# Optimization experiments

Hardware: AMD Instinct MI355X
Metric: run time of the kernel (lower is better)

## Reference

```python
import jax, jax.numpy as jnp
import numpy as np

B, L, D, H = 2, 2048, 1024, 16
HD = D // H

def setup_inputs() -> dict:
    key = jax.random.key(0)
    ks = jax.random.split(key, 9)
    s = 1.0 / np.sqrt(D)
    return {
        "x": jax.random.normal(ks[0], (B, L, D), jnp.float32),
        "Wq": jax.random.normal(ks[1], (D, D), jnp.float32) * s,
        "bq": jax.random.normal(ks[2], (D,), jnp.float32) * 0.02,
        "Wk": jax.random.normal(ks[3], (D, D), jnp.float32) * s,
        "bk": jax.random.normal(ks[4], (D,), jnp.float32) * 0.02,
        "Wv": jax.random.normal(ks[5], (D, D), jnp.float32) * s,
        "bv": jax.random.normal(ks[6], (D,), jnp.float32) * 0.02,
        "Wo": jax.random.normal(ks[7], (D, D), jnp.float32) * s,
        "bo": jax.random.normal(ks[8], (D,), jnp.float32) * 0.02,
    }

def reference(x, Wq, bq, Wk, bk, Wv, bv, Wo, bo):
    b, l, d = x.shape
    # projections -> [B, H, L, HD]
    def split_heads(t):
        return t.reshape(b, l, H, HD).transpose(0, 2, 1, 3)
    Q = split_heads(x @ Wq + bq)
    K = split_heads(x @ Wk + bk)
    V = split_heads(x @ Wv + bv)
    scores = jnp.einsum('bhqd,bhkd->bhqk', Q, K)  # [B,H,L,L]
    causal = jnp.tril(jnp.ones((l, l), bool))
    scores = jnp.where(causal, scores, -jnp.inf)
    attn = jax.nn.softmax(scores / np.sqrt(HD), axis=-1)
    ctx = jnp.einsum('bhqk,bhkd->bhqd', attn, V)
    ctx = ctx.transpose(0, 2, 1, 3).reshape(b, l, d)
    return ctx @ Wo + bo
```

## Files before the change

kernel.cpp:

```cpp
#include <hip/hip_runtime.h>
#include <stdint.h>

typedef unsigned short u16;
typedef __attribute__((ext_vector_type(8))) __bf16 bf16x8;
typedef __attribute__((ext_vector_type(4))) float f32x4;
typedef __attribute__((ext_vector_type(16))) float f32x16;

__device__ __forceinline__ u16 f2bf(float f) {
  union { float f; uint32_t u; } c; c.f = f;
  uint32_t u = c.u + 0x7fffu + ((c.u >> 16) & 1u);
  return (u16)(u >> 16);
}
__device__ __forceinline__ uint32_t cvtpk(float a, float b) {
  uint32_t r;
  asm("v_cvt_pk_bf16_f32 %0, %1, %2" : "=v"(r) : "v"(a), "v"(b));
  return r;
}

__device__ __forceinline__ void async16(const u16* g, u16* l) {
  __builtin_amdgcn_global_load_lds(
      (const __attribute__((address_space(1))) void*)g,
      (__attribute__((address_space(3))) void*)l, 16, 0, 0);
}

__device__ __forceinline__ f32x4 mfma16(bf16x8 a, bf16x8 b, f32x4 c) {
  return __builtin_amdgcn_mfma_f32_16x16x32_bf16(a, b, c, 0, 0, 0);
}
__device__ __forceinline__ f32x16 mfma32(bf16x8 a, bf16x8 b, f32x16 c) {
  return __builtin_amdgcn_mfma_f32_32x32x16_bf16(a, b, c, 0, 0, 0);
}


__global__ __launch_bounds__(256) void x_cvt_kernel(const float* __restrict__ x,
                                                    u16* __restrict__ xb) {
  int i = (blockIdx.x * 256 + threadIdx.x) * 4;
  float4 v = *(const float4*)(x + i);
  uint2 t; t.x = cvtpk(v.x, v.y); t.y = cvtpk(v.z, v.w);
  *(uint2*)(xb + i) = t;
}

__global__ __launch_bounds__(256) void wt_cvt_kernel(const float* __restrict__ Wq,
                                                     const float* __restrict__ Wk,
                                                     const float* __restrict__ Wv,
                                                     const float* __restrict__ Wo,
                                                     u16* __restrict__ out) {
  __shared__ __align__(16) u16 t[64][72];
  int z = blockIdx.z;
  const float* W = (z == 0) ? Wq : (z == 1) ? Wk : (z == 2) ? Wv : Wo;
  u16* o = out + (size_t)z * (1u << 20);
  int n0 = blockIdx.x * 64, k0 = blockIdx.y * 64;
  int tid = threadIdx.x;
  int c4 = (tid & 15) * 4, r0 = tid >> 4;
#pragma unroll
  for (int i = 0; i < 4; i++) {
    int r = r0 + i * 16;
    float4 v = *(const float4*)(W + (size_t)(k0 + r) * 1024 + n0 + c4);
    t[c4 + 0][r] = f2bf(v.x);
    t[c4 + 1][r] = f2bf(v.y);
    t[c4 + 2][r] = f2bf(v.z);
    t[c4 + 3][r] = f2bf(v.w);
  }
  __syncthreads();
  int n = tid >> 2, kc = (tid & 3) * 16;
  uint4 a = *(const uint4*)&t[n][kc];
  uint4 b = *(const uint4*)&t[n][kc + 8];
  *(uint4*)(o + (size_t)(n0 + n) * 1024 + k0 + kc) = a;
  *(uint4*)(o + (size_t)(n0 + n) * 1024 + k0 + kc + 8) = b;
}

template <int TN>
__device__ __forceinline__ void gemm_core2(const u16* __restrict__ A,
                                           const u16* __restrict__ Bt,
                                           u16* As, u16* Bs,
                                           f32x4 (&acc)[4][TN / 32]) {
  constexpr int NJ = TN / 32;
  constexpr int ASZ = 128 * 32, BSZ = TN * 32;
  const int tid = threadIdx.x, wave = tid >> 6, lane = tid & 63;
  const int low = lane & 15, hi = lane >> 4;
  const int wm = wave >> 1, wn = wave & 1;
  const int m0 = blockIdx.y * 128, n0 = blockIdx.x * TN;
  const f32x4 fzero = {0.f, 0.f, 0.f, 0.f};
#pragma unroll
  for (int i = 0; i < 4; i++)
#pragma unroll
    for (int j = 0; j < NJ; j++) acc[i][j] = fzero;

  const int ea0 = wave * 128 + lane, ea1 = ea0 + 64;
  const u16* ga0 = A + (size_t)(m0 + (ea0 >> 2)) * 1024 + (ea0 & 3) * 8;
  const u16* ga1 = A + (size_t)(m0 + (ea1 >> 2)) * 1024 + (ea1 & 3) * 8;
  u16* la0 = As + (wave * 2 + 0) * 512;
  u16* la1 = As + (wave * 2 + 1) * 512;

  const int eb0 = (TN == 128) ? (wave * 128 + lane) : (wave * 64 + lane);
  const int eb1 = eb0 + 64;
  const u16* gb0 = Bt + (size_t)(n0 + (eb0 >> 2)) * 1024 + (eb0 & 3) * 8;
  const u16* gb1 = Bt + (size_t)(n0 + (eb1 >> 2)) * 1024 + (eb1 & 3) * 8;
  u16* lb0 = Bs + ((TN == 128) ? (wave * 2 + 0) * 512 : wave * 512);
  u16* lb1 = Bs + (wave * 2 + 1) * 512;

  const u16* ap = As + (wm * 64 + low) * 32 + hi * 8;
  const u16* bp = Bs + (wn * (TN / 2) + low) * 32 + hi * 8;

#define GSTAGE(buf, KT)                                                        \
  {                                                                            \
    async16(ga0 + (KT), la0 + (buf) * ASZ);                                    \
    async16(ga1 + (KT), la1 + (buf) * ASZ);                                    \
    async16(gb0 + (KT), lb0 + (buf) * BSZ);                                    \
    if (TN == 128) async16(gb1 + (KT), lb1 + (buf) * BSZ);                     \
  }

  GSTAGE(0, 0)
  __syncthreads();
  int buf = 0;
  for (int kt = 0; kt < 1024; kt += 32) {
    if (kt + 32 < 1024) GSTAGE(buf ^ 1, kt + 32)
    bf16x8 af[4], bfv[NJ];
#pragma unroll
    for (int i = 0; i < 4; i++)
      af[i] = *(const bf16x8*)(ap + buf * ASZ + i * 16 * 32);
#pragma unroll
    for (int j = 0; j < NJ; j++)
      bfv[j] = *(const bf16x8*)(bp + buf * BSZ + j * 16 * 32);
#pragma unroll
    for (int i = 0; i < 4; i++)
#pragma unroll
      for (int j = 0; j < NJ; j++) acc[i][j] = mfma16(af[i], bfv[j], acc[i][j]);
    __syncthreads();
    buf ^= 1;
  }
#undef GSTAGE
}

__global__ __launch_bounds__(256) void gemm_qkv_kernel(
    const u16* __restrict__ xb, const u16* __restrict__ wT,
    const float* __restrict__ bq, const float* __restrict__ bk,
    const float* __restrict__ bv,
    u16* __restrict__ qs, u16* __restrict__ ks, u16* __restrict__ vts) {
  __shared__ __align__(16) u16 smem[17440];
  u16* As = smem;
  u16* Bs = smem + 8192;
  const int z = blockIdx.z;
  const u16* Bt = wT + (size_t)z * (1u << 20);
  f32x4 acc[4][4];
  gemm_core2<128>(xb, Bt, As, Bs, acc);

  const float* bias = (z == 0) ? bq : (z == 1) ? bk : bv;
  u16* out = (z == 0) ? qs : (z == 1) ? ks : vts;
  const float scale = (z == 0) ? 0.180336880f : 1.0f;
  const int tid = threadIdx.x, wave = tid >> 6, lane = tid & 63;
  const int low = lane & 15, hi = lane >> 4;
  const int wm = wave >> 1, wn = wave & 1;
  const int m0 = blockIdx.y * 128, n0 = blockIdx.x * 128;

  const int h = (n0 >> 6) + wn;
  const int gmb = m0 + wm * 64;
  const int b = gmb >> 11;
  const int lb = gmb & 2047;

  u16* tile = smem + wave * 4360;
#pragma unroll
  for (int i = 0; i < 4; i++)
#pragma unroll
    for (int j = 0; j < 4; j++) {
      int hd = j * 16 + low;
      float bval = bias[h * 64 + hd];
#pragma unroll
      for (int r = 0; r < 4; r++) {
        int row = i * 16 + hi * 4 + r;
        tile[row * 68 + hd] = f2bf((acc[i][j][r] + bval) * scale);
      }
    }

  if (z != 2) {
    u16* dst = out + ((size_t)((b * 16 + h) * 2048 + lb + lane)) * 64;
    const u16* src = tile + lane * 68;
#pragma unroll
    for (int c = 0; c < 4; c++) {
      uint2 a0 = *(const uint2*)(src + c * 16 + 0);
      uint2 a1 = *(const uint2*)(src + c * 16 + 4);
      uint2 a2 = *(const uint2*)(src + c * 16 + 8);
      uint2 a3 = *(const uint2*)(src + c * 16 + 12);
      uint4 w0; w0.x = a0.x; w0.y = a0.y; w0.z = a1.x; w0.w = a1.y;
      uint4 w1; w1.x = a2.x; w1.y = a2.y; w1.z = a3.x; w1.w = a3.y;
      *(uint4*)(dst + c * 16 + 0) = w0;
      *(uint4*)(dst + c * 16 + 8) = w1;
    }
  } else {
    int l4 = (lane & 15) * 4;
    int lp4 = (l4 & ~12) | ((l4 & 4) << 1) | ((l4 & 8) >> 1);
    int ghd = lane >> 4;
    u16* vbase = out + ((size_t)(b * 16 + h) * 64) * 2048 + lb + lp4;
#pragma unroll
    for (int s = 0; s < 16; s++) {
      int hd = s * 4 + ghd;
      uint32_t v0 = tile[(l4 + 0) * 68 + hd];
      uint32_t v1 = tile[(l4 + 1) * 68 + hd];
      uint32_t v2 = tile[(l4 + 2) * 68 + hd];
      uint32_t v3 = tile[(l4 + 3) * 68 + hd];
      uint2 w; w.x = v0 | (v1 << 16); w.y = v2 | (v3 << 16);
      *(uint2*)(vbase + (size_t)hd * 2048) = w;
    }
  }
}

__global__ __launch_bounds__(256) void gemm_out_kernel(
    const u16* __restrict__ ctx, const u16* __restrict__ woT,
    const float* __restrict__ bo, float* __restrict__ out) {
  __shared__ __align__(16) u16 As[2 * 128 * 32];
  __shared__ __align__(16) u16 Bs[2 * 64 * 32];
  f32x4 acc[4][2];
  gemm_core2<64>(ctx, woT, As, Bs, acc);
  const int tid = threadIdx.x, wave = tid >> 6, lane = tid & 63;
  const int low = lane & 15, hi = lane >> 4;
  const int wm = wave >> 1, wn = wave & 1;
  const int m0 = blockIdx.y * 128, n0 = blockIdx.x * 64;
#pragma unroll
  for (int i = 0; i < 4; i++)
#pragma unroll
    for (int j = 0; j < 2; j++) {
      int gn = n0 + wn * 32 + j * 16 + low;
      float bval = bo[gn];
#pragma unroll
      for (int r = 0; r < 4; r++) {
        int gm = m0 + wm * 64 + i * 16 + hi * 4 + r;
        out[(size_t)gm * 1024 + gn] = acc[i][j][r] + bval;
      }
    }
}

__global__ __launch_bounds__(512) void flash_kernel(
    const u16* __restrict__ Qs, const u16* __restrict__ Ks,
    const u16* __restrict__ Vts, u16* __restrict__ ctx) {
  __shared__ __align__(16) u16 Kls[2][2][64 * 64];
  __shared__ __align__(16) u16 Vls[2][2][64 * 64];

  const int bid = blockIdx.x;
  const int qt = (bid < 256) ? (15 - (bid >> 5)) : ((bid - 256) >> 5);
  const int bh = bid & 31;
  const int qb = qt * 128;
  const int nT = qt + 1;

  const int tid = threadIdx.x, wave = tid >> 6, lane = tid & 63;
  const int wq = wave & 3, g = wave >> 2;
  const int q32 = lane & 31, hi2 = lane >> 5;
  const int x7 = q32 & 7;

  const u16* Qb = Qs + (size_t)bh * (2048 * 64);
  const u16* Kb = Ks + (size_t)bh * (2048 * 64);
  const u16* Vb = Vts + (size_t)bh * (64 * 2048);

  const int qrow = qb + wq * 32 + q32;
  bf16x8 qf[4];
#pragma unroll
  for (int ds = 0; ds < 4; ds++)
    qf[ds] = *(const bf16x8*)(Qb + (size_t)qrow * 64 + ds * 16 + hi2 * 8);

  f32x16 o0, o1;
#pragma unroll
  for (int r = 0; r < 16; r++) { o0[r] = 0.f; o1[r] = 0.f; }
  float m_ = -1e30f, l_ = 0.f;

#define STAGE(buf, KT0)                                                        \
  {                                                                            \
    _Pragma("unroll") for (int i = 0; i < 2; i++) {                            \
      int row = (wq * 2 + i) * 8 + (lane >> 3);                                \
      async16(Kb + (size_t)((KT0) + row) * 64 +                                \
                  (((lane & 7) ^ (row & 7)) * 8),                              \
              &Kls[g][buf][(wq * 2 + i) * 512]);                               \
      async16(Vb + (size_t)row * 2048 + (KT0) +                                \
                  (((lane & 7) ^ (row & 7)) * 8),                              \
              &Vls[g][buf][(wq * 2 + i) * 512]);                               \
    }                                                                          \
  }

  const int tb = g * nT;
  STAGE(0, (tb + 0) * 64)
  STAGE(1, (tb + 1) * 64)

  const int qmax = qb + wq * 32 + 31;

  int cur = 0;
  for (int t = 0; t < nT; t++) {
    const int kt0 = (tb + t) * 64;
    if (t + 1 < nT) { asm volatile("s_waitcnt vmcnt(4)" ::: "memory"); }
    else            { asm volatile("s_waitcnt vmcnt(0)" ::: "memory"); }
    __builtin_amdgcn_s_barrier();

    if (kt0 <= qmax) {
      const u16* Kc = &Kls[g][cur][0];
      const u16* Vc = &Vls[g][cur][0];

      f32x16 s0, s1;
#pragma unroll
      for (int r = 0; r < 16; r++) { s0[r] = 0.f; s1[r] = 0.f; }
      __builtin_amdgcn_s_setprio(1);
#pragma unroll
      for (int ds = 0; ds < 4; ds++) {
        int cs = ((ds * 2 + hi2) ^ x7) * 8;
        bf16x8 kf0 = *(const bf16x8*)(Kc + q32 * 64 + cs);
        bf16x8 kf1 = *(const bf16x8*)(Kc + (32 + q32) * 64 + cs);
        s0 = mfma32(kf0, qf[ds], s0);
        s1 = mfma32(kf1, qf[ds], s1);
      }
      __builtin_amdgcn_s_setprio(0);

      bf16x8 vf0[4], vf1[4];
#pragma unroll
      for (int ksx = 0; ksx < 4; ksx++) {
        int sc = ((2 * ksx + hi2) ^ x7) * 8;
        vf0[ksx] = *(const bf16x8*)(Vc + q32 * 64 + sc);
        vf1[ksx] = *(const bf16x8*)(Vc + (32 + q32) * 64 + sc);
      }

      if (kt0 + 63 > qb + wq * 32) {
#pragma unroll
        for (int r = 0; r < 16; r++) {
          int kl = (r & 3) + 8 * (r >> 2) + 4 * hi2;
          if (kt0 + kl > qrow) s0[r] = -1e30f;
          if (kt0 + 32 + kl > qrow) s1[r] = -1e30f;
        }
      }

      float pm = -1e30f;
#pragma unroll
      for (int r = 0; r < 16; r++) pm = fmaxf(pm, fmaxf(s0[r], s1[r]));
      pm = fmaxf(pm, __shfl_xor(pm, 32));
      if (__any(pm > m_ + 8.f)) {
        float mn = fmaxf(m_, pm);
        float corr = __builtin_amdgcn_exp2f(m_ - mn);
        m_ = mn;
        l_ *= corr;
#pragma unroll
        for (int r = 0; r < 16; r++) { o0[r] *= corr; o1[r] *= corr; }
      }

      float rs = 0.f;
#pragma unroll
      for (int r = 0; r < 16; r++) {
        s0[r] = __builtin_amdgcn_exp2f(s0[r] - m_);
        s1[r] = __builtin_amdgcn_exp2f(s1[r] - m_);
        rs += s0[r] + s1[r];
      }
      rs += __shfl_xor(rs, 32);
      l_ += rs;

      bf16x8 pb[4];
#pragma unroll
      for (int ksx = 0; ksx < 4; ksx++) {
        union { uint32_t u[4]; bf16x8 v; } pu;
        if (ksx < 2) {
          int rb = 8 * ksx;
          pu.u[0] = cvtpk(s0[rb + 0], s0[rb + 1]);
          pu.u[1] = cvtpk(s0[rb + 2], s0[rb + 3]);
          pu.u[2] = cvtpk(s0[rb + 4], s0[rb + 5]);
          pu.u[3] = cvtpk(s0[rb + 6], s0[rb + 7]);
        } else {
          int rb = 8 * (ksx - 2);
          pu.u[0] = cvtpk(s1[rb + 0], s1[rb + 1]);
          pu.u[1] = cvtpk(s1[rb + 2], s1[rb + 3]);
          pu.u[2] = cvtpk(s1[rb + 4], s1[rb + 5]);
          pu.u[3] = cvtpk(s1[rb + 6], s1[rb + 7]);
        }
        pb[ksx] = pu.v;
      }

      __builtin_amdgcn_s_setprio(1);
#pragma unroll
      for (int ksx = 0; ksx < 4; ksx++) {
        o0 = mfma32(vf0[ksx], pb[ksx], o0);
        o1 = mfma32(vf1[ksx], pb[ksx], o1);
      }
      __builtin_amdgcn_s_setprio(0);
    }

    __builtin_amdgcn_s_barrier();
    if (t + 2 < nT) STAGE(cur, (tb + t + 2) * 64)
    cur ^= 1;
  }

  __syncthreads();
  float* mb = (float*)&Kls[0][0][0] + wq * 2304;
  if (g == 1) {
#pragma unroll
    for (int m = 0; m < 4; m++) {
      f32x4 qa = {o0[4 * m + 0], o0[4 * m + 1], o0[4 * m + 2], o0[4 * m + 3]};
      f32x4 qb2 = {o1[4 * m + 0], o1[4 * m + 1], o1[4 * m + 2], o1[4 * m + 3]};
      *(f32x4*)(mb + m * 256 + (lane << 2)) = qa;
      *(f32x4*)(mb + (4 + m) * 256 + (lane << 2)) = qb2;
    }
    mb[2048 + (lane << 1) + 0] = m_;
    mb[2048 + (lane << 1) + 1] = l_;
  }
  __syncthreads();
  if (g == 0) {
    float m1 = mb[2048 + (lane << 1) + 0];
    float l1 = mb[2048 + (lane << 1) + 1];
    float mm = fmaxf(m_, m1);
    float cA = __builtin_amdgcn_exp2f(m_ - mm);
    float cB = __builtin_amdgcn_exp2f(m1 - mm);
    l_ = l_ * cA + l1 * cB;
#pragma unroll
    for (int m = 0; m < 4; m++) {
      f32x4 qa = *(const f32x4*)(mb + m * 256 + (lane << 2));
      f32x4 qb2 = *(const f32x4*)(mb + (4 + m) * 256 + (lane << 2));
#pragma unroll
      for (int j = 0; j < 4; j++) {
        o0[4 * m + j] = o0[4 * m + j] * cA + qa[j] * cB;
        o1[4 * m + j] = o1[4 * m + j] * cA + qb2[j] * cB;
      }
    }

    const int b = bh >> 4, h = bh & 15;
    float inv = 1.f / l_;
    size_t base = ((size_t)(b * 2048 + qrow)) * 1024 + h * 64;
#pragma unroll
    for (int m = 0; m < 4; m++) {
      uint2 w0, w1;
      w0.x = cvtpk(o0[4 * m + 0] * inv, o0[4 * m + 1] * inv);
      w0.y = cvtpk(o0[4 * m + 2] * inv, o0[4 * m + 3] * inv);
      *(uint2*)(ctx + base + 8 * m + 4 * hi2) = w0;
      w1.x = cvtpk(o1[4 * m + 0] * inv, o1[4 * m + 1] * inv);
      w1.y = cvtpk(o1[4 * m + 2] * inv, o1[4 * m + 3] * inv);
      *(uint2*)(ctx + base + 32 + 8 * m + 4 * hi2) = w1;
    }
  }
}


extern "C" void kernel_launch(void* const* d_in, const int* in_sizes, int n_in,
                              void* d_out, int out_size, void* d_ws, size_t ws_size,
                              hipStream_t stream) {
  const float* x  = (const float*)d_in[0];
  const float* Wq = (const float*)d_in[1];
  const float* bq = (const float*)d_in[2];
  const float* Wk = (const float*)d_in[3];
  const float* bk = (const float*)d_in[4];
  const float* Wv = (const float*)d_in[5];
  const float* bv = (const float*)d_in[6];
  const float* Wo = (const float*)d_in[7];
  const float* bo = (const float*)d_in[8];

  char* ws = (char*)d_ws;
  u16* xb  = (u16*)(ws);
  u16* wT  = (u16*)(ws + (8u << 20));
  u16* qs  = (u16*)(ws + (16u << 20));
  u16* ks  = (u16*)(ws + (24u << 20));
  u16* vts = (u16*)(ws + (32u << 20));
  u16* ctx = (u16*)(ws + (40u << 20));

  x_cvt_kernel<<<4096, 256, 0, stream>>>(x, xb);
  wt_cvt_kernel<<<dim3(16, 16, 4), 256, 0, stream>>>(Wq, Wk, Wv, Wo, wT);
  gemm_qkv_kernel<<<dim3(8, 32, 3), 256, 0, stream>>>(xb, wT, bq, bk, bv, qs, ks, vts);
  flash_kernel<<<512, 512, 0, stream>>>(qs, ks, vts, ctx);
  gemm_out_kernel<<<dim3(16, 32), 256, 0, stream>>>(ctx, wT + 3 * (1u << 20), bo, (float*)d_out);
}
```

Measured before the change: 118.4 us.

## Split flash attention KV range across four wave groups with 1024-thread blocks

Doubles the flash kernel block to 1024 threads so four wave groups split each query tile's KV tiles, instead of two groups taking contiguous halves. Tiles are assigned round-robin, and out-of-range prefetches are clamped to the last tile. Partial outputs from groups 1-3 are merged into group 0 through shared memory. The per-tile row-sum cross-lane shuffle is deferred to the end, max and sum use tree reductions, and the block order for the second half of the grid changes. The aim is more parallelism per query tile and a shorter serial KV loop. The cost is a larger LDS footprint, a tighter per-thread register budget at 1024 threads, and a bigger final merge.

```diff
diff --git a/kernel.cpp b/kernel.cpp
--- a/kernel.cpp
+++ b/kernel.cpp
@@ -228,17 +228,17 @@
     }
 }
 
-__global__ __launch_bounds__(512) void flash_kernel(
+__global__ __launch_bounds__(1024) void flash_kernel(
     const u16* __restrict__ Qs, const u16* __restrict__ Ks,
     const u16* __restrict__ Vts, u16* __restrict__ ctx) {
-  __shared__ __align__(16) u16 Kls[2][2][64 * 64];
-  __shared__ __align__(16) u16 Vls[2][2][64 * 64];
+  __shared__ __align__(16) u16 smem[65536];
 
   const int bid = blockIdx.x;
-  const int qt = (bid < 256) ? (15 - (bid >> 5)) : ((bid - 256) >> 5);
+  const int qt = (bid < 256) ? (15 - (bid >> 5)) : (7 - ((bid - 256) >> 5));
   const int bh = bid & 31;
   const int qb = qt * 128;
-  const int nT = qt + 1;
+  const int nkv = 2 * qt + 2;
+  const int loopN = (nkv + 3) >> 2;
 
   const int tid = threadIdx.x, wave = tid >> 6, lane = tid & 63;
   const int wq = wave & 3, g = wave >> 2;
@@ -259,6 +259,9 @@
 #pragma unroll
   for (int r = 0; r < 16; r++) { o0[r] = 0.f; o1[r] = 0.f; }
   float m_ = -1e30f, l_ = 0.f;
+
+  u16* Kg = smem + g * 8192;
+  u16* Vg = smem + 32768 + g * 8192;
 
 #define STAGE(buf, KT0)                                                        \
   {                                                                            \
@@ -266,29 +269,33 @@
       int row = (wq * 2 + i) * 8 + (lane >> 3);                                \
       async16(Kb + (size_t)((KT0) + row) * 64 +                                \
                   (((lane & 7) ^ (row & 7)) * 8),                              \
-              &Kls[g][buf][(wq * 2 + i) * 512]);                               \
+              Kg + (buf) * 4096 + (wq * 2 + i) * 512);                         \
       async16(Vb + (size_t)row * 2048 + (KT0) +                                \
                   (((lane & 7) ^ (row & 7)) * 8),                              \
-              &Vls[g][buf][(wq * 2 + i) * 512]);                               \
+              Vg + (buf) * 4096 + (wq * 2 + i) * 512);                         \
     }                                                                          \
   }
 
-  const int tb = g * nT;
-  STAGE(0, (tb + 0) * 64)
-  STAGE(1, (tb + 1) * 64)
+  const int Tmax = nkv - 1;
+  {
+    int T0 = (g < nkv) ? g : Tmax;
+    int T1 = (4 + g < nkv) ? (4 + g) : Tmax;
+    STAGE(0, T0 * 64)
+    STAGE(1, T1 * 64)
+  }
 
   const int qmax = qb + wq * 32 + 31;
 
   int cur = 0;
-  for (int t = 0; t < nT; t++) {
-    const int kt0 = (tb + t) * 64;
-    if (t + 1 < nT) { asm volatile("s_waitcnt vmcnt(4)" ::: "memory"); }
-    else            { asm volatile("s_waitcnt vmcnt(0)" ::: "memory"); }
+  for (int t = 0; t < loopN; t++) {
+    const int kt0 = (4 * t + g) * 64;
+    if (t + 1 < loopN) { asm volatile("s_waitcnt vmcnt(4)" ::: "memory"); }
+    else               { asm volatile("s_waitcnt vmcnt(0)" ::: "memory"); }
     __builtin_amdgcn_s_barrier();
 
     if (kt0 <= qmax) {
-      const u16* Kc = &Kls[g][cur][0];
-      const u16* Vc = &Vls[g][cur][0];
+      const u16* Kc = Kg + cur * 4096;
+      const u16* Vc = Vg + cur * 4096;
 
       f32x16 s0, s1;
 #pragma unroll
@@ -321,9 +328,15 @@
         }
       }
 
-      float pm = -1e30f;
-#pragma unroll
-      for (int r = 0; r < 16; r++) pm = fmaxf(pm, fmaxf(s0[r], s1[r]));
+      float t16[16];
+#pragma unroll
+      for (int r = 0; r < 16; r++) t16[r] = fmaxf(s0[r], s1[r]);
+#pragma unroll
+      for (int w = 8; w >= 1; w >>= 1)
+#pragma unroll
+        for (int i = 0; i < 8; i++)
+          if (i < w) t16[i] = fmaxf(t16[i], t16[i + w]);
+      float pm = t16[0];
       pm = fmaxf(pm, __shfl_xor(pm, 32));
       if (__any(pm > m_ + 8.f)) {
         float mn = fmaxf(m_, pm);
@@ -334,15 +347,19 @@
         for (int r = 0; r < 16; r++) { o0[r] *= corr; o1[r] *= corr; }
       }
 
-      float rs = 0.f;
+      float a16[16];
 #pragma unroll
       for (int r = 0; r < 16; r++) {
         s0[r] = __builtin_amdgcn_exp2f(s0[r] - m_);
         s1[r] = __builtin_amdgcn_exp2f(s1[r] - m_);
-        rs += s0[r] + s1[r];
-      }
-      rs += __shfl_xor(rs, 32);
-      l_ += rs;
+        a16[r] = s0[r] + s1[r];
+      }
+#pragma unroll
+      for (int w = 8; w >= 1; w >>= 1)
+#pragma unroll
+        for (int i = 0; i < 8; i++)
+          if (i < w) a16[i] += a16[i + w];
+      l_ += a16[0];
 
       bf16x8 pb[4];
 #pragma unroll
@@ -374,13 +391,17 @@
     }
 
     __builtin_amdgcn_s_barrier();
-    if (t + 2 < nT) STAGE(cur, (tb + t + 2) * 64)
+    if (t + 2 < loopN) {
+      int Tn = 4 * (t + 2) + g;
+      if (Tn > Tmax) Tn = Tmax;
+      STAGE(cur, Tn * 64)
+    }
     cur ^= 1;
   }
 
   __syncthreads();
-  float* mb = (float*)&Kls[0][0][0] + wq * 2304;
-  if (g == 1) {
+  float* mb = (float*)smem + (wq * 3 + (g - 1)) * 2176;
+  if (g >= 1) {
 #pragma unroll
     for (int m = 0; m < 4; m++) {
       f32x4 qa = {o0[4 * m + 0], o0[4 * m + 1], o0[4 * m + 2], o0[4 * m + 3]};
@@ -393,25 +414,31 @@
   }
   __syncthreads();
   if (g == 0) {
-    float m1 = mb[2048 + (lane << 1) + 0];
-    float l1 = mb[2048 + (lane << 1) + 1];
-    float mm = fmaxf(m_, m1);
-    float cA = __builtin_amdgcn_exp2f(m_ - mm);
-    float cB = __builtin_amdgcn_exp2f(m1 - mm);
-    l_ = l_ * cA + l1 * cB;
-#pragma unroll
-    for (int m = 0; m < 4; m++) {
-      f32x4 qa = *(const f32x4*)(mb + m * 256 + (lane << 2));
-      f32x4 qb2 = *(const f32x4*)(mb + (4 + m) * 256 + (lane << 2));
-#pragma unroll
-      for (int j = 0; j < 4; j++) {
-        o0[4 * m + j] = o0[4 * m + j] * cA + qa[j] * cB;
-        o1[4 * m + j] = o1[4 * m + j] * cA + qb2[j] * cB;
-      }
-    }
-
+#pragma unroll
+    for (int gs = 1; gs < 4; gs++) {
+      float* ms = (float*)smem + (wq * 3 + (gs - 1)) * 2176;
+      float m1 = ms[2048 + (lane << 1) + 0];
+      float l1 = ms[2048 + (lane << 1) + 1];
+      float mm = fmaxf(m_, m1);
+      float cA = __builtin_amdgcn_exp2f(m_ - mm);
+      float cB = __builtin_amdgcn_exp2f(m1 - mm);
+      m_ = mm;
+      l_ = l_ * cA + l1 * cB;
+#pragma unroll
+      for (int m = 0; m < 4; m++) {
+        f32x4 qa = *(const f32x4*)(ms + m * 256 + (lane << 2));
+        f32x4 qb2 = *(const f32x4*)(ms + (4 + m) * 256 + (lane << 2));
+#pragma unroll
+        for (int j = 0; j < 4; j++) {
+          o0[4 * m + j] = o0[4 * m + j] * cA + qa[j] * cB;
+          o1[4 * m + j] = o1[4 * m + j] * cA + qb2[j] * cB;
+        }
+      }
+    }
+
+    float lrow = l_ + __shfl_xor(l_, 32);
     const int b = bh >> 4, h = bh & 15;
-    float inv = 1.f / l_;
+    float inv = 1.f / lrow;
     size_t base = ((size_t)(b * 2048 + qrow)) * 1024 + h * 64;
 #pragma unroll
     for (int m = 0; m < 4; m++) {
@@ -451,6 +478,6 @@
   x_cvt_kernel<<<4096, 256, 0, stream>>>(x, xb);
   wt_cvt_kernel<<<dim3(16, 16, 4), 256, 0, stream>>>(Wq, Wk, Wv, Wo, wT);
   gemm_qkv_kernel<<<dim3(8, 32, 3), 256, 0, stream>>>(xb, wT, bq, bk, bv, qs, ks, vts);
-  flash_kernel<<<512, 512, 0, stream>>>(qs, ks, vts, ctx);
+  flash_kernel<<<512, 1024, 0, stream>>>(qs, ks, vts, ctx);
   gemm_out_kernel<<<dim3(16, 32), 256, 0, stream>>>(ctx, wT + 3 * (1u << 20), bo, (float*)d_out);
 }
```

Result: slower. 141.5 us (+19.5%).

## Load K and V tiles straight from global memory, dropping LDS double buffering

Applied to the files above, without the earlier changes.

Removes the async global-to-LDS staging of K and V tiles, along with the double buffer, waitcnt and barriers. Each wave now reads its K rows and V^T rows directly from global memory into registers. Because no barriers remain in the loop, waves can exit as soon as their causal range ends. The trade-off is that the four q-waves of each group each read the same K/V tile separately from global/L2, with no async prefetch to hide the latency.

```diff
diff --git a/kernel.cpp b/kernel.cpp
--- a/kernel.cpp
+++ b/kernel.cpp
@@ -231,8 +231,7 @@
 __global__ __launch_bounds__(512) void flash_kernel(
     const u16* __restrict__ Qs, const u16* __restrict__ Ks,
     const u16* __restrict__ Vts, u16* __restrict__ ctx) {
-  __shared__ __align__(16) u16 Kls[2][2][64 * 64];
-  __shared__ __align__(16) u16 Vls[2][2][64 * 64];
+  __shared__ __align__(16) float msc[4][2304];
 
   const int bid = blockIdx.x;
   const int qt = (bid < 256) ? (15 - (bid >> 5)) : ((bid - 256) >> 5);
@@ -243,7 +242,6 @@
   const int tid = threadIdx.x, wave = tid >> 6, lane = tid & 63;
   const int wq = wave & 3, g = wave >> 2;
   const int q32 = lane & 31, hi2 = lane >> 5;
-  const int x7 = q32 & 7;
 
   const u16* Qb = Qs + (size_t)bh * (2048 * 64);
   const u16* Kb = Ks + (size_t)bh * (2048 * 64);
@@ -260,126 +258,103 @@
   for (int r = 0; r < 16; r++) { o0[r] = 0.f; o1[r] = 0.f; }
   float m_ = -1e30f, l_ = 0.f;
 
-#define STAGE(buf, KT0)                                                        \
-  {                                                                            \
-    _Pragma("unroll") for (int i = 0; i < 2; i++) {                            \
-      int row = (wq * 2 + i) * 8 + (lane >> 3);                                \
-      async16(Kb + (size_t)((KT0) + row) * 64 +                                \
-                  (((lane & 7) ^ (row & 7)) * 8),                              \
-              &Kls[g][buf][(wq * 2 + i) * 512]);                               \
-      async16(Vb + (size_t)row * 2048 + (KT0) +                                \
-                  (((lane & 7) ^ (row & 7)) * 8),                              \
-              &Vls[g][buf][(wq * 2 + i) * 512]);                               \
-    }                                                                          \
-  }
-
   const int tb = g * nT;
-  STAGE(0, (tb + 0) * 64)
-  STAGE(1, (tb + 1) * 64)
-
   const int qmax = qb + wq * 32 + 31;
 
-  int cur = 0;
+  const u16* vr0 = Vb + (size_t)q32 * 2048;
+  const u16* vr1 = Vb + (size_t)(32 + q32) * 2048;
+
   for (int t = 0; t < nT; t++) {
     const int kt0 = (tb + t) * 64;
-    if (t + 1 < nT) { asm volatile("s_waitcnt vmcnt(4)" ::: "memory"); }
-    else            { asm volatile("s_waitcnt vmcnt(0)" ::: "memory"); }
-    __builtin_amdgcn_s_barrier();
-
-    if (kt0 <= qmax) {
-      const u16* Kc = &Kls[g][cur][0];
-      const u16* Vc = &Vls[g][cur][0];
-
-      f32x16 s0, s1;
-#pragma unroll
-      for (int r = 0; r < 16; r++) { s0[r] = 0.f; s1[r] = 0.f; }
-      __builtin_amdgcn_s_setprio(1);
-#pragma unroll
-      for (int ds = 0; ds < 4; ds++) {
-        int cs = ((ds * 2 + hi2) ^ x7) * 8;
-        bf16x8 kf0 = *(const bf16x8*)(Kc + q32 * 64 + cs);
-        bf16x8 kf1 = *(const bf16x8*)(Kc + (32 + q32) * 64 + cs);
-        s0 = mfma32(kf0, qf[ds], s0);
-        s1 = mfma32(kf1, qf[ds], s1);
+    if (kt0 > qmax) break;
+
+    const u16* kr0 = Kb + (size_t)(kt0 + q32) * 64;
+    const u16* kr1 = Kb + (size_t)(kt0 + 32 + q32) * 64;
+    f32x16 s0, s1;
+#pragma unroll
+    for (int r = 0; r < 16; r++) { s0[r] = 0.f; s1[r] = 0.f; }
+    __builtin_amdgcn_s_setprio(1);
+#pragma unroll
+    for (int ds = 0; ds < 4; ds++) {
+      int cs = (2 * ds + hi2) * 8;
+      bf16x8 kf0 = *(const bf16x8*)(kr0 + cs);
+      bf16x8 kf1 = *(const bf16x8*)(kr1 + cs);
+      s0 = mfma32(kf0, qf[ds], s0);
+      s1 = mfma32(kf1, qf[ds], s1);
+    }
+    __builtin_amdgcn_s_setprio(0);
+
+    bf16x8 vf0[4], vf1[4];
+#pragma unroll
+    for (int ksx = 0; ksx < 4; ksx++) {
+      int sc = (2 * ksx + hi2) * 8;
+      vf0[ksx] = *(const bf16x8*)(vr0 + kt0 + sc);
+      vf1[ksx] = *(const bf16x8*)(vr1 + kt0 + sc);
+    }
+
+    if (kt0 + 63 > qb + wq * 32) {
+#pragma unroll
+      for (int r = 0; r < 16; r++) {
+        int kl = (r & 3) + 8 * (r >> 2) + 4 * hi2;
+        if (kt0 + kl > qrow) s0[r] = -1e30f;
+        if (kt0 + 32 + kl > qrow) s1[r] = -1e30f;
       }
-      __builtin_amdgcn_s_setprio(0);
-
-      bf16x8 vf0[4], vf1[4];
-#pragma unroll
-      for (int ksx = 0; ksx < 4; ksx++) {
-        int sc = ((2 * ksx + hi2) ^ x7) * 8;
-        vf0[ksx] = *(const bf16x8*)(Vc + q32 * 64 + sc);
-        vf1[ksx] = *(const bf16x8*)(Vc + (32 + q32) * 64 + sc);
+    }
+
+    float pm = -1e30f;
+#pragma unroll
+    for (int r = 0; r < 16; r++) pm = fmaxf(pm, fmaxf(s0[r], s1[r]));
+    pm = fmaxf(pm, __shfl_xor(pm, 32));
+    if (__any(pm > m_ + 8.f)) {
+      float mn = fmaxf(m_, pm);
+      float corr = __builtin_amdgcn_exp2f(m_ - mn);
+      m_ = mn;
+      l_ *= corr;
+#pragma unroll
+      for (int r = 0; r < 16; r++) { o0[r] *= corr; o1[r] *= corr; }
+    }
+
+    float rs = 0.f;
+#pragma unroll
+    for (int r = 0; r < 16; r++) {
+      s0[r] = __builtin_amdgcn_exp2f(s0[r] - m_);
+      s1[r] = __builtin_amdgcn_exp2f(s1[r] - m_);
+      rs += s0[r] + s1[r];
+    }
+    rs += __shfl_xor(rs, 32);
+    l_ += rs;
+
+    bf16x8 pb[4];
+#pragma unroll
+    for (int ksx = 0; ksx < 4; ksx++) {
+      union { uint32_t u[4]; bf16x8 v; } pu;
+      if (ksx < 2) {
+        int rb = 8 * ksx;
+        pu.u[0] = cvtpk(s0[rb + 0], s0[rb + 1]);
+        pu.u[1] = cvtpk(s0[rb + 2], s0[rb + 3]);
+        pu.u[2] = cvtpk(s0[rb + 4], s0[rb + 5]);
+        pu.u[3] = cvtpk(s0[rb + 6], s0[rb + 7]);
+      } else {
+        int rb = 8 * (ksx - 2);
+        pu.u[0] = cvtpk(s1[rb + 0], s1[rb + 1]);
+        pu.u[1] = cvtpk(s1[rb + 2], s1[rb + 3]);
+        pu.u[2] = cvtpk(s1[rb + 4], s1[rb + 5]);
+        pu.u[3] = cvtpk(s1[rb + 6], s1[rb + 7]);
       }
-
-      if (kt0 + 63 > qb + wq * 32) {
-#pragma unroll
-        for (int r = 0; r < 16; r++) {
-          int kl = (r & 3) + 8 * (r >> 2) + 4 * hi2;
-          if (kt0 + kl > qrow) s0[r] = -1e30f;
-          if (kt0 + 32 + kl > qrow) s1[r] = -1e30f;
-        }
-      }
-
-      float pm = -1e30f;
-#pragma unroll
-      for (int r = 0; r < 16; r++) pm = fmaxf(pm, fmaxf(s0[r], s1[r]));
-      pm = fmaxf(pm, __shfl_xor(pm, 32));
-      if (__any(pm > m_ + 8.f)) {
-        float mn = fmaxf(m_, pm);
-        float corr = __builtin_amdgcn_exp2f(m_ - mn);
-        m_ = mn;
-        l_ *= corr;
-#pragma unroll
-        for (int r = 0; r < 16; r++) { o0[r] *= corr; o1[r] *= corr; }
-      }
-
-      float rs = 0.f;
-#pragma unroll
-      for (int r = 0; r < 16; r++) {
-        s0[r] = __builtin_amdgcn_exp2f(s0[r] - m_);
-        s1[r] = __builtin_amdgcn_exp2f(s1[r] - m_);
-        rs += s0[r] + s1[r];
-      }
-      rs += __shfl_xor(rs, 32);
-      l_ += rs;
-
-      bf16x8 pb[4];
-#pragma unroll
-      for (int ksx = 0; ksx < 4; ksx++) {
-        union { uint32_t u[4]; bf16x8 v; } pu;
-        if (ksx < 2) {
-          int rb = 8 * ksx;
-          pu.u[0] = cvtpk(s0[rb + 0], s0[rb + 1]);
-          pu.u[1] = cvtpk(s0[rb + 2], s0[rb + 3]);
-          pu.u[2] = cvtpk(s0[rb + 4], s0[rb + 5]);
-          pu.u[3] = cvtpk(s0[rb + 6], s0[rb + 7]);
-        } else {
-          int rb = 8 * (ksx - 2);
-          pu.u[0] = cvtpk(s1[rb + 0], s1[rb + 1]);
-          pu.u[1] = cvtpk(s1[rb + 2], s1[rb + 3]);
-          pu.u[2] = cvtpk(s1[rb + 4], s1[rb + 5]);
-          pu.u[3] = cvtpk(s1[rb + 6], s1[rb + 7]);
-        }
-        pb[ksx] = pu.v;
-      }
-
-      __builtin_amdgcn_s_setprio(1);
-#pragma unroll
-      for (int ksx = 0; ksx < 4; ksx++) {
-        o0 = mfma32(vf0[ksx], pb[ksx], o0);
-        o1 = mfma32(vf1[ksx], pb[ksx], o1);
-      }
-      __builtin_amdgcn_s_setprio(0);
-    }
-
-    __builtin_amdgcn_s_barrier();
-    if (t + 2 < nT) STAGE(cur, (tb + t + 2) * 64)
-    cur ^= 1;
+      pb[ksx] = pu.v;
+    }
+
+    __builtin_amdgcn_s_setprio(1);
+#pragma unroll
+    for (int ksx = 0; ksx < 4; ksx++) {
+      o0 = mfma32(vf0[ksx], pb[ksx], o0);
+      o1 = mfma32(vf1[ksx], pb[ksx], o1);
+    }
+    __builtin_amdgcn_s_setprio(0);
   }
 
   __syncthreads();
-  float* mb = (float*)&Kls[0][0][0] + wq * 2304;
+  float* mb = msc[wq];
   if (g == 1) {
 #pragma unroll
     for (int m = 0; m < 4; m++) {
```

Result: slower. 156.9 us (+32.6%).
